# Kernel optimization log

Hardware: AMD Instinct MI355X
Metric: run time of the kernel (lower is better)

## Reference

```python
import jax, jax.numpy as jnp
import numpy as np

B, S, E = 2, 8192, 128


def setup_inputs() -> dict:
    key = jax.random.key(0)
    ks = jax.random.split(key, 7)
    sc = 1.0 / np.sqrt(E)
    return {
        "x": jax.random.normal(ks[0], (B, S, E), dtype=jnp.float32),
        "Wq": jax.random.normal(ks[1], (E, E), dtype=jnp.float32) * sc,
        "bq": jax.random.normal(ks[2], (E,), dtype=jnp.float32) * 0.01,
        "Wk": jax.random.normal(ks[3], (E, E), dtype=jnp.float32) * sc,
        "bk": jax.random.normal(ks[4], (E,), dtype=jnp.float32) * 0.01,
        "Wv": jax.random.normal(ks[5], (E, E), dtype=jnp.float32) * sc,
        "bv": jax.random.normal(ks[6], (E,), dtype=jnp.float32) * 0.01,
    }


def reference(x, Wq, bq, Wk, bk, Wv, bv):
    # x: [B, S, E]. Conv1d(k=1) == per-slice linear: out[b,s,o] = sum_e W[o,e] x[b,s,e] + b[o]
    embed_dim = x.shape[-1]
    Q = jnp.einsum("bse,oe->bso", x, Wq) + bq  # [B, S, E]
    K = jnp.einsum("bse,oe->bso", x, Wk) + bk
    V = jnp.einsum("bse,oe->bso", x, Wv) + bv
    scores = jnp.einsum("bsd,btd->bst", Q, K) / jnp.sqrt(
        jnp.asarray(embed_dim, dtype=x.dtype)
    )  # [B, S, S]
    A = jax.nn.softmax(scores, axis=-1)
    # torch: out = bmm(V^T_as[B,E,S], A^T)[.transpose] == sum_t A[b,s,t] V[b,t,e]
    out = jnp.einsum("bst,bte->bse", A, V)  # [B, S, E]
    return out
```

## Files before the change

kernel.cpp:

```cpp
#include <hip/hip_runtime.h>
#include <math.h>

#define NB 2
#define NS 8192
#define NE 128
#define NROWS (NB * NS)

typedef __attribute__((ext_vector_type(8))) short s8v;
typedef __attribute__((ext_vector_type(16))) float fx16;
typedef __attribute__((ext_vector_type(2))) unsigned int u2v;
typedef __attribute__((address_space(1))) const unsigned char as1c;
typedef __attribute__((address_space(3))) unsigned char as3t;

static __device__ __forceinline__ unsigned int pkbf(float a, float b) {
    unsigned int ua = __float_as_uint(a), ub = __float_as_uint(b);
    ua += 0x7FFFu + ((ua >> 16) & 1u);
    ub += 0x7FFFu + ((ub >> 16) & 1u);
    return (ua >> 16) | (ub & 0xFFFF0000u);
}

static __device__ __forceinline__ unsigned int cvtpk(float a, float b) {
    unsigned int r;
    asm("v_cvt_pk_bf16_f32 %0, %1, %2" : "=v"(r) : "v"(a), "v"(b));
    return r;
}

static __device__ __forceinline__ void split8(const float* p, uint4& H, uint4& L) {
    float4 a = *(const float4*)p;
    float4 b = *(const float4*)(p + 4);
    unsigned int h0 = cvtpk(a.x, a.y), h1 = cvtpk(a.z, a.w);
    unsigned int h2 = cvtpk(b.x, b.y), h3 = cvtpk(b.z, b.w);
    H = make_uint4(h0, h1, h2, h3);
    float l0 = a.x - __uint_as_float(h0 << 16);
    float l1 = a.y - __uint_as_float(h0 & 0xFFFF0000u);
    float l2 = a.z - __uint_as_float(h1 << 16);
    float l3 = a.w - __uint_as_float(h1 & 0xFFFF0000u);
    float l4 = b.x - __uint_as_float(h2 << 16);
    float l5 = b.y - __uint_as_float(h2 & 0xFFFF0000u);
    float l6 = b.z - __uint_as_float(h3 << 16);
    float l7 = b.w - __uint_as_float(h3 & 0xFFFF0000u);
    L = make_uint4(cvtpk(l0, l1), cvtpk(l2, l3), cvtpk(l4, l5), cvtpk(l6, l7));
}

__global__ __launch_bounds__(256, 4)
void split_kernel(const float* __restrict__ x,
                  const float* __restrict__ Wq, const float* __restrict__ Wk,
                  const float* __restrict__ Wv,
                  unsigned short* __restrict__ xh, unsigned short* __restrict__ xl,
                  unsigned short* __restrict__ WhS, unsigned short* __restrict__ WlS)
{
    const int bid = blockIdx.x;
    if (bid < 1024) {
        const int i = (bid * 256 + threadIdx.x) * 8;
        uint4 H, L;
        split8(&x[i], H, L);
        *(uint4*)&xh[i] = H;
        *(uint4*)&xl[i] = L;
    } else {
        const int tid = (bid - 1024) * 256 + threadIdx.x;
        const int mat = tid >> 11;
        const int rem = tid & 2047;
        const int r = rem >> 4, g = rem & 15;
        const float* W = (mat == 0) ? Wq : (mat == 1) ? Wk : Wv;
        uint4 H, L;
        split8(&W[r * 128 + g * 8], H, L);
        const int gs = g ^ (r & 7);
        *(uint4*)&WhS[mat * 16384 + r * 128 + gs * 8] = H;
        *(uint4*)&WlS[mat * 16384 + r * 128 + gs * 8] = L;
    }
}

__global__ __launch_bounds__(256, 3)
void qkv_kernel(const unsigned short* __restrict__ xh,
                const unsigned short* __restrict__ xl,
                const unsigned short* __restrict__ WhS,
                const unsigned short* __restrict__ WlS,
                const float* __restrict__ bq, const float* __restrict__ bk,
                const float* __restrict__ bv,
                unsigned short* __restrict__ qkv)
{
    __shared__ unsigned short WhL[64 * 128];
    __shared__ unsigned short WlL[64 * 128];

    const int t    = threadIdx.x;
    const int rblk = blockIdx.x * 128;
    const int mat  = blockIdx.y;
    const int o0   = blockIdx.z * 64;

    const float* bias = (mat == 0) ? bq : (mat == 1) ? bk : bv;
    unsigned short* out = qkv + (size_t)mat * NROWS * NE;
    const float osc = (mat == 0) ? 0.1275174460620886f : 1.0f;

    {
        const unsigned short* hsrc = WhS + mat * 16384 + o0 * 128;
        const unsigned short* lsrc = WlS + mat * 16384 + o0 * 128;
        #pragma unroll
        for (int p = 0; p < 4; ++p) {
            __builtin_amdgcn_global_load_lds((as1c*)(hsrc + p * 2048 + t * 8),
                (as3t*)&WhL[p * 2048 + t * 8], 16, 0, 0);
            __builtin_amdgcn_global_load_lds((as1c*)(lsrc + p * 2048 + t * 8),
                (as3t*)&WlL[p * 2048 + t * 8], 16, 0, 0);
        }
    }

    const int w = t >> 6, lane = t & 63, lq = lane & 31, h = lane >> 5;
    const int rw = rblk + w * 32;

    s8v xhf[8], xlf[8];
    #pragma unroll
    for (int s = 0; s < 8; ++s) {
        xhf[s] = *(const s8v*)(xh + (size_t)(rw + lq) * NE + s * 16 + h * 8);
        xlf[s] = *(const s8v*)(xl + (size_t)(rw + lq) * NE + s * 16 + h * 8);
    }

    __syncthreads();

    fx16 acc[2];
    #pragma unroll
    for (int ot = 0; ot < 2; ++ot)
        #pragma unroll
        for (int i = 0; i < 16; ++i) acc[ot][i] = 0.f;

    #pragma unroll
    for (int s = 0; s < 8; ++s) {
        #pragma unroll
        for (int ot = 0; ot < 2; ++ot) {
            const int co = ((s * 2 + h) ^ (lq & 7)) * 8;
            s8v wh = *(const s8v*)&WhL[(ot * 32 + lq) * 128 + co];
            s8v wl = *(const s8v*)&WlL[(ot * 32 + lq) * 128 + co];
            if (mat != 2) {
                acc[ot] = __builtin_amdgcn_mfma_f32_32x32x16_bf16(wh, xhf[s], acc[ot], 0, 0, 0);
                acc[ot] = __builtin_amdgcn_mfma_f32_32x32x16_bf16(wh, xlf[s], acc[ot], 0, 0, 0);
                acc[ot] = __builtin_amdgcn_mfma_f32_32x32x16_bf16(wl, xhf[s], acc[ot], 0, 0, 0);
            } else {
                acc[ot] = __builtin_amdgcn_mfma_f32_32x32x16_bf16(xhf[s], wh, acc[ot], 0, 0, 0);
                acc[ot] = __builtin_amdgcn_mfma_f32_32x32x16_bf16(xlf[s], wh, acc[ot], 0, 0, 0);
                acc[ot] = __builtin_amdgcn_mfma_f32_32x32x16_bf16(xhf[s], wl, acc[ot], 0, 0, 0);
            }
        }
    }

    if (mat != 2) {
        const size_t rbase = (size_t)(rw + lq) * NE;
        #pragma unroll
        for (int ot = 0; ot < 2; ++ot)
            #pragma unroll
            for (int g = 0; g < 4; ++g) {
                int ob = o0 + ot * 32 + 4 * h + 8 * g;
                float4 bb = *(const float4*)&bias[ob];
                float v0 = (acc[ot][4 * g + 0] + bb.x) * osc;
                float v1 = (acc[ot][4 * g + 1] + bb.y) * osc;
                float v2 = (acc[ot][4 * g + 2] + bb.z) * osc;
                float v3 = (acc[ot][4 * g + 3] + bb.w) * osc;
                *(uint2*)&out[rbase + ob] = make_uint2(pkbf(v0, v1), pkbf(v2, v3));
            }
    } else {
        const int bb_ = rw >> 13, kb = (rw & (NS - 1)) + 4 * h;
        #pragma unroll
        for (int ot = 0; ot < 2; ++ot) {
            int o = o0 + ot * 32 + lq;
            float bv_ = bias[o];
            size_t obase = ((size_t)(bb_ * NE + o) << 13) + kb;
            #pragma unroll
            for (int g = 0; g < 4; ++g) {
                float v0 = acc[ot][4 * g + 0] + bv_;
                float v1 = acc[ot][4 * g + 1] + bv_;
                float v2 = acc[ot][4 * g + 2] + bv_;
                float v3 = acc[ot][4 * g + 3] + bv_;
                *(uint2*)&out[obase + 8 * g] = make_uint2(pkbf(v0, v1), pkbf(v2, v3));
            }
        }
    }
}

__global__ __launch_bounds__(256, 2)
void attn_kernel(const unsigned short* __restrict__ qkv,
                 _Float16* __restrict__ pd,
                 _Float16* __restrict__ pw,
                 float* __restrict__ ml)
{
    __shared__ unsigned short kbuf[2][64 * 128];
    __shared__ unsigned short vbuf[2][64 * 128];

    const int t  = threadIdx.x;
    const int id = blockIdx.x;
    const int ks = id & 3;
    const int b  = (id >> 2) & 1;
    const int T  = id >> 3;

    const unsigned short* Qg = qkv;
    const unsigned short* Kg = qkv + (size_t)NROWS * NE;
    const unsigned short* Vb = qkv + (size_t)2 * NROWS * NE + ((size_t)b << 20);

    const int w = t >> 6, lane = t & 63, lq = lane & 31, h = lane >> 5;
    const int qbw = b * NS + T * 128 + w * 32;
    const size_t kvb = (size_t)b * NS * NE;
    const int kq0 = ks * 2048;

    s8v qf[8];
    #pragma unroll
    for (int s = 0; s < 8; ++s)
        qf[s] = *(const s8v*)(Qg + (size_t)(qbw + lq) * NE + s * 16 + h * 8);

    fx16 acc[4];
    #pragma unroll
    for (int dt = 0; dt < 4; ++dt)
        #pragma unroll
        for (int i = 0; i < 16; ++i) acc[dt][i] = 0.f;

    float l = 0.f;

    const unsigned short* gptr[8];
    if (w < 2) {
        #pragma unroll
        for (int j = 0; j < 8; ++j) {
            int i = 8 * w + j;
            int keyl = 4 * i + (lane >> 4);
            int c = (lane & 15) ^ (keyl & 7);
            gptr[j] = Kg + kvb + (size_t)(kq0 + keyl) * NE + c * 8;
        }
    } else {
        #pragma unroll
        for (int j = 0; j < 8; ++j) {
            int i = 8 * (w - 2) + j;
            int d = 8 * i + (lane >> 3);
            int g = (lane & 7) ^ (d & 7);
            gptr[j] = Vb + ((size_t)d << 13) + kq0 + g * 8;
        }
    }
    const int gstride = (w < 2) ? 64 * NE : 64;

    auto stage = [&](int bufi) {
        if (w < 2) {
            #pragma unroll
            for (int j = 0; j < 8; ++j) {
                __builtin_amdgcn_global_load_lds((as1c*)gptr[j],
                    (as3t*)&kbuf[bufi][(8 * w + j) * 512], 16, 0, 0);
                gptr[j] += gstride;
            }
        } else {
            #pragma unroll
            for (int j = 0; j < 8; ++j) {
                __builtin_amdgcn_global_load_lds((as1c*)gptr[j],
                    (as3t*)&vbuf[bufi][(8 * (w - 2) + j) * 512], 16, 0, 0);
                gptr[j] += gstride;
            }
        }
    };

    stage(0);
    __syncthreads();

#define PEX(i) (st2[(i) >> 4][(i) & 15])
    int buf = 0;
    const int swz = (lq & 7) * 8;

    for (int r = 0; r < 32; ++r) {
        if (r < 31) stage(buf ^ 1);

        fx16 st2[2];
        #pragma unroll
        for (int mt = 0; mt < 2; ++mt)
            #pragma unroll
            for (int i = 0; i < 16; ++i) st2[mt][i] = 0.f;
        __builtin_amdgcn_s_setprio(1);
        #pragma unroll
        for (int s = 0; s < 8; ++s) {
            int co = ((s * 2 + h) * 8) ^ swz;
            s8v a0 = *(const s8v*)&kbuf[buf][lq * 128 + co];
            s8v a1 = *(const s8v*)&kbuf[buf][(32 + lq) * 128 + co];
            st2[0] = __builtin_amdgcn_mfma_f32_32x32x16_bf16(a0, qf[s], st2[0], 0, 0, 0);
            st2[1] = __builtin_amdgcn_mfma_f32_32x32x16_bf16(a1, qf[s], st2[1], 0, 0, 0);
        }
        __builtin_amdgcn_s_setprio(0);

        float a0s = 0.f, a1s = 0.f, a2s = 0.f, a3s = 0.f;
        #pragma unroll
        for (int i = 0; i < 32; i += 4) {
            PEX(i)     = __builtin_amdgcn_exp2f(PEX(i));
            PEX(i + 1) = __builtin_amdgcn_exp2f(PEX(i + 1));
            PEX(i + 2) = __builtin_amdgcn_exp2f(PEX(i + 2));
            PEX(i + 3) = __builtin_amdgcn_exp2f(PEX(i + 3));
            a0s += PEX(i); a1s += PEX(i + 1); a2s += PEX(i + 2); a3s += PEX(i + 3);
        }
        float lsum = (a0s + a1s) + (a2s + a3s);
        lsum += __shfl_xor(lsum, 32);
        l += lsum;

        #pragma unroll
        for (int s2 = 0; s2 < 4; ++s2) {
            unsigned int P0 = cvtpk(PEX(s2 * 8 + 0), PEX(s2 * 8 + 1));
            unsigned int P1 = cvtpk(PEX(s2 * 8 + 2), PEX(s2 * 8 + 3));
            unsigned int P2 = cvtpk(PEX(s2 * 8 + 4), PEX(s2 * 8 + 5));
            unsigned int P3 = cvtpk(PEX(s2 * 8 + 6), PEX(s2 * 8 + 7));
            u2v r02 = __builtin_amdgcn_permlane32_swap(P0, P2, false, false);
            u2v r13 = __builtin_amdgcn_permlane32_swap(P1, P3, false, false);
            union { unsigned int u[4]; s8v v; } pf;
            pf.u[0] = r02.x;
            pf.u[1] = r13.x;
            pf.u[2] = r02.y;
            pf.u[3] = r13.y;
            int go = ((s2 * 2 + h) * 8) ^ swz;
            __builtin_amdgcn_s_setprio(1);
            #pragma unroll
            for (int dt = 0; dt < 4; ++dt) {
                s8v vf = *(const s8v*)&vbuf[buf][(lq + 32 * dt) * 64 + go];
                acc[dt] = __builtin_amdgcn_mfma_f32_32x32x16_bf16(pf.v, vf, acc[dt], 0, 0, 0);
            }
            __builtin_amdgcn_s_setprio(0);
        }

        __syncthreads();
        buf ^= 1;
    }
#undef PEX

    if (lane < 32)
        ml[(size_t)(qbw + lq) * 4 + ks] = l;

    float invl = 1.0f / l;
    _Float16* P = (ks < 2) ? pd : pw;
    const int slot = (ks & 1) * 128;
    #pragma unroll
    for (int rg = 0; rg < 16; ++rg) {
        int row = (rg & 3) + 8 * (rg >> 2) + 4 * h;
        float sc = __shfl(invl, row);
        size_t rb = (size_t)(qbw + row) * 256 + slot;
        #pragma unroll
        for (int dt = 0; dt < 4; ++dt)
            P[rb + lq + 32 * dt] = (_Float16)(acc[dt][rg] * sc);
    }
}

__global__ __launch_bounds__(256, 2)
void merge_kernel(const _Float16* __restrict__ pw,
                  const float* __restrict__ ml,
                  float* __restrict__ outp)
{
    const int gi = blockIdx.x * 256 + threadIdx.x;
    const int q = gi >> 4, d0 = (gi & 15) * 8;
    const _Float16* pd = (const _Float16*)outp;

    uint4 u0 = *(const uint4*)&pd[(size_t)q * 256 + d0];
    uint4 u1 = *(const uint4*)&pd[(size_t)q * 256 + 128 + d0];
    uint4 u2 = *(const uint4*)&pw[(size_t)q * 256 + d0];
    uint4 u3 = *(const uint4*)&pw[(size_t)q * 256 + 128 + d0];
    float l0 = ml[q * 4 + 0], l1 = ml[q * 4 + 1];
    float l2 = ml[q * 4 + 2], l3 = ml[q * 4 + 3];

    float inv = 1.f / (l0 + l1 + l2 + l3);
    float a0 = l0 * inv, a1 = l1 * inv, a2 = l2 * inv, a3 = l3 * inv;

    union { uint4 u; _Float16 hh[8]; } c0, c1, c2, c3;
    c0.u = u0; c1.u = u1; c2.u = u2; c3.u = u3;
    float ov[8];
    #pragma unroll
    for (int e = 0; e < 8; ++e)
        ov[e] = (float)c0.hh[e] * a0 + (float)c1.hh[e] * a1 +
                (float)c2.hh[e] * a2 + (float)c3.hh[e] * a3;

    *(float4*)&outp[(size_t)q * 128 + d0]     = *(float4*)&ov[0];
    *(float4*)&outp[(size_t)q * 128 + d0 + 4] = *(float4*)&ov[4];
}

extern "C" void kernel_launch(void* const* d_in, const int* in_sizes, int n_in,
                              void* d_out, int out_size, void* d_ws, size_t ws_size,
                              hipStream_t stream)
{
    const float* x  = (const float*)d_in[0];
    const float* Wq = (const float*)d_in[1];
    const float* bq = (const float*)d_in[2];
    const float* Wk = (const float*)d_in[3];
    const float* bk = (const float*)d_in[4];
    const float* Wv = (const float*)d_in[5];
    const float* bv = (const float*)d_in[6];
    float* out = (float*)d_out;

    unsigned char* ws = (unsigned char*)d_ws;
    unsigned short* qkv = (unsigned short*)ws;
    _Float16* pw = (_Float16*)(ws + (size_t)3 * NROWS * NE * 2);
    float* mlp = (float*)(ws + (size_t)3 * NROWS * NE * 2
                             + (size_t)NROWS * 256 * 2);
    unsigned char* ws2 = ws + (size_t)3 * NROWS * NE * 2
                            + (size_t)NROWS * 256 * 2 + (size_t)NROWS * 16;
    unsigned short* xh  = (unsigned short*)ws2;
    unsigned short* xl  = xh + (size_t)NROWS * NE;
    unsigned short* WhS = xl + (size_t)NROWS * NE;
    unsigned short* WlS = WhS + 3 * NE * NE;

    split_kernel<<<1048, 256, 0, stream>>>(x, Wq, Wk, Wv, xh, xl, WhS, WlS);

    dim3 g1(NROWS / 128, 3, 2);
    qkv_kernel<<<g1, 256, 0, stream>>>(xh, xl, WhS, WlS, bq, bk, bv, qkv);

    attn_kernel<<<512, 256, 0, stream>>>(qkv, (_Float16*)d_out, pw, mlp);
    merge_kernel<<<1024, 256, 0, stream>>>(pw, mlp, out);
}
```

Measured before the change: 165.2 us.

## Stage x tiles in LDS and transpose QKV output through shared memory

The QKV projection kernel now loads both the x hi/lo tiles and the weight tiles into swizzled LDS with global_load_lds, using 64-row blocks where each wave computes one 32x32 output tile. Results are staged through a padded LDS buffer so Q/K/V stores become coalesced 16-byte row writes, including the transposed V layout. Before, x came straight from global memory and each thread wrote scattered 8-byte values. In exchange the grid doubles, LDS use per block grows, and the occupancy hint drops from 3 to 2.

Result: no change. 164.1 us (-0.7%).

```diff
diff --git a/kernel.cpp b/kernel.cpp
--- a/kernel.cpp
+++ b/kernel.cpp
@@ -70,7 +70,7 @@
     }
 }
 
-__global__ __launch_bounds__(256, 3)
+__global__ __launch_bounds__(256, 2)
 void qkv_kernel(const unsigned short* __restrict__ xh,
                 const unsigned short* __restrict__ xl,
                 const unsigned short* __restrict__ WhS,
@@ -79,11 +79,13 @@
                 const float* __restrict__ bv,
                 unsigned short* __restrict__ qkv)
 {
+    __shared__ unsigned short xhL[64 * 128];
+    __shared__ unsigned short xlL[64 * 128];
     __shared__ unsigned short WhL[64 * 128];
     __shared__ unsigned short WlL[64 * 128];
 
     const int t    = threadIdx.x;
-    const int rblk = blockIdx.x * 128;
+    const int rblk = blockIdx.x * 64;
     const int mat  = blockIdx.y;
     const int o0   = blockIdx.z * 64;
 
@@ -91,84 +93,106 @@
     unsigned short* out = qkv + (size_t)mat * NROWS * NE;
     const float osc = (mat == 0) ? 0.1275174460620886f : 1.0f;
 
-    {
-        const unsigned short* hsrc = WhS + mat * 16384 + o0 * 128;
-        const unsigned short* lsrc = WlS + mat * 16384 + o0 * 128;
-        #pragma unroll
-        for (int p = 0; p < 4; ++p) {
-            __builtin_amdgcn_global_load_lds((as1c*)(hsrc + p * 2048 + t * 8),
-                (as3t*)&WhL[p * 2048 + t * 8], 16, 0, 0);
-            __builtin_amdgcn_global_load_lds((as1c*)(lsrc + p * 2048 + t * 8),
-                (as3t*)&WlL[p * 2048 + t * 8], 16, 0, 0);
-        }
-    }
-
     const int w = t >> 6, lane = t & 63, lq = lane & 31, h = lane >> 5;
-    const int rw = rblk + w * 32;
-
-    s8v xhf[8], xlf[8];
+
+    if (w < 2) {
+        const unsigned short* src = (w == 0) ? xh : xl;
+        unsigned short* dst = (w == 0) ? xhL : xlL;
+        const int rb4 = lane >> 4;
+        const int cg  = lane & 15;
+        #pragma unroll
+        for (int i = 0; i < 16; ++i) {
+            const int row = 4 * i + rb4;
+            const int c   = cg ^ (row & 7);
+            __builtin_amdgcn_global_load_lds(
+                (as1c*)(src + (size_t)(rblk + row) * NE + c * 8),
+                (as3t*)(dst + i * 512 + lane * 8), 16, 0, 0);
+        }
+    } else {
+        const unsigned short* src = ((w == 2) ? WhS : WlS) + mat * 16384 + o0 * 128;
+        unsigned short* dst = (w == 2) ? WhL : WlL;
+        #pragma unroll
+        for (int i = 0; i < 16; ++i) {
+            __builtin_amdgcn_global_load_lds(
+                (as1c*)(src + i * 512 + lane * 8),
+                (as3t*)(dst + i * 512 + lane * 8), 16, 0, 0);
+        }
+    }
+    __syncthreads();
+
+    const int rloc = (w & 1) * 32;
+    const int ot   = w >> 1;
+
+    s8v xhf[8], xlf[8], whf[8], wlf[8];
     #pragma unroll
     for (int s = 0; s < 8; ++s) {
-        xhf[s] = *(const s8v*)(xh + (size_t)(rw + lq) * NE + s * 16 + h * 8);
-        xlf[s] = *(const s8v*)(xl + (size_t)(rw + lq) * NE + s * 16 + h * 8);
+        const int cx = ((s * 2 + h) ^ (lq & 7)) * 8;
+        xhf[s] = *(const s8v*)&xhL[(rloc + lq) * 128 + cx];
+        xlf[s] = *(const s8v*)&xlL[(rloc + lq) * 128 + cx];
+        whf[s] = *(const s8v*)&WhL[(ot * 32 + lq) * 128 + cx];
+        wlf[s] = *(const s8v*)&WlL[(ot * 32 + lq) * 128 + cx];
+    }
+
+    fx16 acc;
+    #pragma unroll
+    for (int i = 0; i < 16; ++i) acc[i] = 0.f;
+
+    #pragma unroll
+    for (int s = 0; s < 8; ++s) {
+        if (mat != 2) {
+            acc = __builtin_amdgcn_mfma_f32_32x32x16_bf16(whf[s], xhf[s], acc, 0, 0, 0);
+            acc = __builtin_amdgcn_mfma_f32_32x32x16_bf16(whf[s], xlf[s], acc, 0, 0, 0);
+            acc = __builtin_amdgcn_mfma_f32_32x32x16_bf16(wlf[s], xhf[s], acc, 0, 0, 0);
+        } else {
+            acc = __builtin_amdgcn_mfma_f32_32x32x16_bf16(xhf[s], whf[s], acc, 0, 0, 0);
+            acc = __builtin_amdgcn_mfma_f32_32x32x16_bf16(xlf[s], whf[s], acc, 0, 0, 0);
+            acc = __builtin_amdgcn_mfma_f32_32x32x16_bf16(xhf[s], wlf[s], acc, 0, 0, 0);
+        }
     }
 
     __syncthreads();
-
-    fx16 acc[2];
-    #pragma unroll
-    for (int ot = 0; ot < 2; ++ot)
-        #pragma unroll
-        for (int i = 0; i < 16; ++i) acc[ot][i] = 0.f;
-
-    #pragma unroll
-    for (int s = 0; s < 8; ++s) {
-        #pragma unroll
-        for (int ot = 0; ot < 2; ++ot) {
-            const int co = ((s * 2 + h) ^ (lq & 7)) * 8;
-            s8v wh = *(const s8v*)&WhL[(ot * 32 + lq) * 128 + co];
-            s8v wl = *(const s8v*)&WlL[(ot * 32 + lq) * 128 + co];
-            if (mat != 2) {
-                acc[ot] = __builtin_amdgcn_mfma_f32_32x32x16_bf16(wh, xhf[s], acc[ot], 0, 0, 0);
-                acc[ot] = __builtin_amdgcn_mfma_f32_32x32x16_bf16(wh, xlf[s], acc[ot], 0, 0, 0);
-                acc[ot] = __builtin_amdgcn_mfma_f32_32x32x16_bf16(wl, xhf[s], acc[ot], 0, 0, 0);
-            } else {
-                acc[ot] = __builtin_amdgcn_mfma_f32_32x32x16_bf16(xhf[s], wh, acc[ot], 0, 0, 0);
-                acc[ot] = __builtin_amdgcn_mfma_f32_32x32x16_bf16(xlf[s], wh, acc[ot], 0, 0, 0);
-                acc[ot] = __builtin_amdgcn_mfma_f32_32x32x16_bf16(xhf[s], wl, acc[ot], 0, 0, 0);
-            }
-        }
-    }
+    unsigned short* TB = xhL;
 
     if (mat != 2) {
-        const size_t rbase = (size_t)(rw + lq) * NE;
-        #pragma unroll
-        for (int ot = 0; ot < 2; ++ot)
-            #pragma unroll
-            for (int g = 0; g < 4; ++g) {
-                int ob = o0 + ot * 32 + 4 * h + 8 * g;
-                float4 bb = *(const float4*)&bias[ob];
-                float v0 = (acc[ot][4 * g + 0] + bb.x) * osc;
-                float v1 = (acc[ot][4 * g + 1] + bb.y) * osc;
-                float v2 = (acc[ot][4 * g + 2] + bb.z) * osc;
-                float v3 = (acc[ot][4 * g + 3] + bb.w) * osc;
-                *(uint2*)&out[rbase + ob] = make_uint2(pkbf(v0, v1), pkbf(v2, v3));
-            }
+        #pragma unroll
+        for (int g = 0; g < 4; ++g) {
+            const int ob = o0 + ot * 32 + 4 * h + 8 * g;
+            float4 bb = *(const float4*)&bias[ob];
+            float v0 = (acc[4 * g + 0] + bb.x) * osc;
+            float v1 = (acc[4 * g + 1] + bb.y) * osc;
+            float v2 = (acc[4 * g + 2] + bb.z) * osc;
+            float v3 = (acc[4 * g + 3] + bb.w) * osc;
+            *(uint2*)&TB[(rloc + lq) * 72 + ot * 32 + 4 * h + 8 * g] =
+                make_uint2(pkbf(v0, v1), pkbf(v2, v3));
+        }
+        __syncthreads();
+        #pragma unroll
+        for (int it = 0; it < 2; ++it) {
+            const int r2 = it * 32 + (t >> 3);
+            const int c2 = (t & 7) * 8;
+            uint4 vv = *(const uint4*)&TB[r2 * 72 + c2];
+            *(uint4*)&out[(size_t)(rblk + r2) * NE + o0 + c2] = vv;
+        }
     } else {
-        const int bb_ = rw >> 13, kb = (rw & (NS - 1)) + 4 * h;
-        #pragma unroll
-        for (int ot = 0; ot < 2; ++ot) {
-            int o = o0 + ot * 32 + lq;
-            float bv_ = bias[o];
-            size_t obase = ((size_t)(bb_ * NE + o) << 13) + kb;
-            #pragma unroll
-            for (int g = 0; g < 4; ++g) {
-                float v0 = acc[ot][4 * g + 0] + bv_;
-                float v1 = acc[ot][4 * g + 1] + bv_;
-                float v2 = acc[ot][4 * g + 2] + bv_;
-                float v3 = acc[ot][4 * g + 3] + bv_;
-                *(uint2*)&out[obase + 8 * g] = make_uint2(pkbf(v0, v1), pkbf(v2, v3));
-            }
+        const float bv_ = bias[o0 + ot * 32 + lq];
+        #pragma unroll
+        for (int g = 0; g < 4; ++g) {
+            float v0 = acc[4 * g + 0] + bv_;
+            float v1 = acc[4 * g + 1] + bv_;
+            float v2 = acc[4 * g + 2] + bv_;
+            float v3 = acc[4 * g + 3] + bv_;
+            *(uint2*)&TB[(ot * 32 + lq) * 72 + rloc + 4 * h + 8 * g] =
+                make_uint2(pkbf(v0, v1), pkbf(v2, v3));
+        }
+        __syncthreads();
+        const int bb_ = rblk >> 13;
+        #pragma unroll
+        for (int it = 0; it < 2; ++it) {
+            const int d2 = it * 32 + (t >> 3);
+            const int kc = (t & 7) * 8;
+            uint4 vv = *(const uint4*)&TB[d2 * 72 + kc];
+            *(uint4*)&out[(((size_t)(bb_ * NE + o0 + d2)) << 13)
+                          + (rblk & (NS - 1)) + kc] = vv;
         }
     }
 }
@@ -390,7 +414,7 @@
 
     split_kernel<<<1048, 256, 0, stream>>>(x, Wq, Wk, Wv, xh, xl, WhS, WlS);
 
-    dim3 g1(NROWS / 128, 3, 2);
+    dim3 g1(NROWS / 64, 3, 2);
     qkv_kernel<<<g1, 256, 0, stream>>>(xh, xl, WhS, WlS, bq, bk, bv, qkv);
 
     attn_kernel<<<512, 256, 0, stream>>>(qkv, (_Float16*)d_out, pw, mlp);
```
